# Kernel tuning notes

Hardware: AMD Instinct MI355X
Metric: run time of the kernel (lower is better)

The kernel has to match this reference:

```python
import jax, jax.numpy as jnp
import numpy as np

# Production dims: NTU-RGB+D skeletons, mid-network AGCN block
N, C, T, V = 64, 64, 300, 25   # batch, channels, frames, joints
S = 3                          # num_subset (spatial partitions of adjacency)
IC = 64 // 4                   # inter_channels = out_channels // coff_embedding
OC = 64                        # out_channels (== in_channels -> down is Identity)
BN_EPS = 1e-5


def setup_inputs() -> dict:
    key = jax.random.key(0)
    ks = jax.random.split(key, 13)
    x = jax.random.normal(ks[0], (N, C, T, V), jnp.float32)
    A = jax.random.uniform(ks[1], (S, V, V), jnp.float32)          # fixed graph buffer
    PA = jax.random.normal(ks[2], (S, V, V), jnp.float32) * 1e-3   # learned adjacency (init ~1e-6)
    wa = jax.random.normal(ks[3], (S, IC, C), jnp.float32) * 0.05  # conv_a 1x1 weights
    ba = jax.random.normal(ks[4], (S, IC), jnp.float32) * 0.01
    wb = jax.random.normal(ks[5], (S, IC, C), jnp.float32) * 0.05  # conv_b 1x1 weights
    bb = jax.random.normal(ks[6], (S, IC), jnp.float32) * 0.01
    wd = jax.random.normal(ks[7], (S, OC, C), jnp.float32) * 0.05  # conv_d 1x1 weights
    bd = jax.random.normal(ks[8], (S, OC), jnp.float32) * 0.01
    bn_gamma = jax.random.uniform(ks[9], (OC,), jnp.float32) + 0.5
    bn_beta = jax.random.normal(ks[10], (OC,), jnp.float32) * 0.1
    bn_mean = jax.random.normal(ks[11], (OC,), jnp.float32) * 0.1
    bn_var = jax.random.uniform(ks[12], (OC,), jnp.float32) + 0.5
    return {"x": x, "A": A, "PA": PA, "wa": wa, "ba": ba, "wb": wb, "bb": bb,
            "wd": wd, "bd": bd, "bn_gamma": bn_gamma, "bn_beta": bn_beta,
            "bn_mean": bn_mean, "bn_var": bn_var}


def reference(x, A, PA, wa, ba, wb, bb, wd, bd, bn_gamma, bn_beta, bn_mean, bn_var):
    n, c, t, v = x.shape
    s, ic, _ = wa.shape
    A_total = A + PA                                                # (S,V,V)

    # conv_a / conv_b are 1x1 convs over channels, vectorized over subsets
    a = jnp.einsum('nctv,skc->nsktv', x, wa) + ba[None, :, :, None, None]  # (N,S,IC,T,V)
    b = jnp.einsum('nctv,skc->nsktv', x, wb) + bb[None, :, :, None, None]

    # attention_a: permute(0,3,1,2).view(N, V, IC*T); attention_b: view(N, IC*T, V)
    a_flat = a.transpose(0, 1, 4, 2, 3).reshape(n, s, v, ic * t)   # (N,S,V,IC*T)
    b_flat = b.reshape(n, s, ic * t, v)                            # (N,S,IC*T,V)

    scores = jnp.einsum('nsvm,nsmu->nsvu', a_flat, b_flat) / (ic * t)
    att = jax.nn.softmax(scores, axis=-2) + A_total[None]          # softmax over dim -2, then + adjacency

    # feature matmul: x.view(N, C*T, V) @ att  ==  contract over node axis v
    y = jnp.einsum('nctv,nsvu->nsctu', x, att)                     # (N,S,C,T,V)
    # conv_d (1x1) per subset, summed over subsets
    z = jnp.einsum('nsctv,soc->notv', y, wd) + jnp.sum(bd, axis=0)[None, :, None, None]

    # BatchNorm2d (inference form with running stats)
    scale = (bn_gamma / jnp.sqrt(bn_var + BN_EPS))[None, :, None, None]
    zn = (z - bn_mean[None, :, None, None]) * scale + bn_beta[None, :, None, None]

    # down is Identity since in_channels == out_channels
    return jax.nn.relu(zn + x)
```

## Files before the change

### kernel.cpp

```cpp
#include <hip/hip_runtime.h>
#include <math.h>


typedef short  short4v  __attribute__((ext_vector_type(4)));
typedef short  short8v  __attribute__((ext_vector_type(8)));
typedef float  float4v  __attribute__((ext_vector_type(4)));

#define MFMA_BF16(a,b,c) __builtin_amdgcn_mfma_f32_16x16x32_bf16((a),(b),(c),0,0,0)

__device__ __forceinline__ unsigned short f2bf(float f) {
  union { float f; unsigned int u; } v; v.f = f;
  unsigned int r = v.u + 0x7FFFu + ((v.u >> 16) & 1u);
  return (unsigned short)(r >> 16);
}
__device__ __forceinline__ unsigned pack2bf(float a, float b) {
#if __has_builtin(__builtin_amdgcn_cvt_pk_bf16_f32)
  typedef __bf16 bf2_t __attribute__((ext_vector_type(2)));
  bf2_t p = __builtin_amdgcn_cvt_pk_bf16_f32(a, b);
  union { bf2_t v; unsigned u; } c; c.v = p; return c.u;
#else
  return (unsigned)f2bf(a) | ((unsigned)f2bf(b) << 16);
#endif
}
__device__ __forceinline__ short8v pk8(const float* f) {
  union { unsigned u[4]; short8v s; } c;
  c.u[0] = pack2bf(f[0], f[1]); c.u[1] = pack2bf(f[2], f[3]);
  c.u[2] = pack2bf(f[4], f[5]); c.u[3] = pack2bf(f[6], f[7]);
  return c.s;
}
__device__ __forceinline__ short8v ld8_b64(const unsigned short* p) {
  short4v a = *(const short4v*)p;
  short4v b = *(const short4v*)(p + 4);
  short8v r;
  r[0]=a[0]; r[1]=a[1]; r[2]=a[2]; r[3]=a[3];
  r[4]=b[0]; r[5]=b[1]; r[6]=b[2]; r[7]=b[3];
  return r;
}

__global__ __launch_bounds__(256) void k0_zero(float* __restrict__ p, int nelem) {
  int i = blockIdx.x * 256 + threadIdx.x;
  if (i < nelem) p[i] = 0.f;
}

__global__ __launch_bounds__(256) void k1_scores(
    const float* __restrict__ x,  const float* __restrict__ wa,
    const float* __restrict__ ba, const float* __restrict__ wb,
    const float* __restrict__ bb, float* __restrict__ scores)
{
  __shared__ __align__(16) unsigned short ET[3][160*40];
  const unsigned tid  = threadIdx.x;
  const unsigned lane = tid & 63u, w = tid >> 6;
  const unsigned l15  = lane & 15u, q = lane >> 4;
  const unsigned n = blockIdx.y, ts = blockIdx.x;
  const unsigned t0 = ts * 12u;
  const float* xn = x + (size_t)n * 480000;

  short8v Wf[3][2][2];
  #pragma unroll
  for (int s = 0; s < 3; ++s)
    #pragma unroll
    for (int mt = 0; mt < 2; ++mt)
      #pragma unroll
      for (int ks = 0; ks < 2; ++ks) {
        const float* src = (mt ? wb : wa) + ((size_t)s*16 + l15)*64
                         + (unsigned)ks*32 + q*8;
        float tf[8];
        #pragma unroll
        for (int j = 0; j < 8; ++j) tf[j] = src[j];
        Wf[s][mt][ks] = pk8(tf);
      }
  float bias[3][2][4];
  #pragma unroll
  for (int s = 0; s < 3; ++s)
    #pragma unroll
    for (int mt = 0; mt < 2; ++mt)
      #pragma unroll
      for (int r = 0; r < 4; ++r)
        bias[s][mt][r] = (mt ? bb : ba)[s*16 + q*4 + (unsigned)r];

  float4v acc[3];
  #pragma unroll
  for (int j = 0; j < 3; ++j) acc[j] = (float4v){0.f,0.f,0.f,0.f};

  for (unsigned ch = 0; ch < 2; ++ch) {
    const unsigned tvbase = (t0 + ch*6u) * 25u;
    if (ch) __syncthreads();
    for (unsigned nn = 0; nn < 3; ++nn) {
      unsigned nt = w + 4*nn;
      if (nt < 10) {
        unsigned tvb = nt*16 + l15;
        unsigned tvg = tvbase + tvb;
        if (tvg > 7499u) tvg = 7499u;
        const float* p = xn + (size_t)q*60000 + tvg;
        float xa[8], xb[8];
        #pragma unroll
        for (int j = 0; j < 8; ++j) {
          xa[j] = p[(size_t)j*7500];
          xb[j] = p[240000 + (size_t)j*7500];
        }
        short8v B0 = pk8(xa), B1 = pk8(xb);
        #pragma unroll
        for (int s = 0; s < 3; ++s)
          #pragma unroll
          for (int mt = 0; mt < 2; ++mt) {
            float4v d = (float4v){0.f,0.f,0.f,0.f};
            d = MFMA_BF16(Wf[s][mt][0], B0, d);
            d = MFMA_BF16(Wf[s][mt][1], B1, d);
            unsigned krb = (unsigned)mt*16 + q*4;
            uint2 pk2;
            pk2.x = pack2bf(d[0] + bias[s][mt][0], d[1] + bias[s][mt][1]);
            pk2.y = pack2bf(d[2] + bias[s][mt][2], d[3] + bias[s][mt][3]);
            *(uint2*)(&ET[s][tvb*40 + krb]) = pk2;
          }
      }
    }
    __syncthreads();
    #pragma unroll
    for (int j = 0; j < 3; ++j) {
      unsigned g = (unsigned)j*4 + w;
      unsigned s = g >> 2, mt = (g >> 1) & 1u, nt2 = g & 1u;
      #pragma unroll
      for (int ks = 0; ks < 3; ++ks) {
        unsigned t    = 2*ks + (q >> 1);
        unsigned kofs = 8*(q & 1u);
        short8v Af = *(const short8v*)(&ET[s][(t*25 + mt*16  + l15)*40 + kofs]);
        short8v Bf = *(const short8v*)(&ET[s][(t*25 + nt2*16 + l15)*40 + 16 + kofs]);
        acc[j] = MFMA_BF16(Af, Bf, acc[j]);
      }
    }
  }
  #pragma unroll
  for (int j = 0; j < 3; ++j) {
    unsigned g = (unsigned)j*4 + w;
    unsigned s = g >> 2, mt = (g >> 1) & 1u, nt2 = g & 1u;
    unsigned u = nt2*16 + l15;
    if (u < 25) {
      #pragma unroll
      for (int r = 0; r < 4; ++r) {
        unsigned v = mt*16 + q*4 + (unsigned)r;
        if (v < 25)
          atomicAdd(&scores[(size_t)n*1875 + s*625 + v*25 + u], acc[j][r]);
      }
    }
  }
}

__global__ __launch_bounds__(64) void k2_softmax(
    const float* __restrict__ scores, const float* __restrict__ A,
    const float* __restrict__ PA, float* __restrict__ att)
{
  const unsigned tid = threadIdx.x, s = blockIdx.x, n = blockIdx.y;
  if (tid >= 25) return;
  const unsigned u = tid;
  float col[25];
  float m = -1e30f;
  #pragma unroll
  for (int v = 0; v < 25; ++v) {
    col[v] = scores[(size_t)n*1875 + s*625 + (unsigned)v*25 + u] * (1.f/4800.f);
    m = fmaxf(m, col[v]);
  }
  float S = 0.f;
  #pragma unroll
  for (int v = 0; v < 25; ++v) { col[v] = expf(col[v] - m); S += col[v]; }
  float inv = 1.f / S;
  #pragma unroll
  for (int v = 0; v < 25; ++v)
    att[(((size_t)n*3 + s)*25 + (unsigned)v)*25 + u] =
        col[v]*inv + A[s*625 + (unsigned)v*25 + u] + PA[s*625 + (unsigned)v*25 + u];
}

__global__ __launch_bounds__(256) void k3_main(
    const float* __restrict__ x,   const float* __restrict__ wd,
    const float* __restrict__ bd,  const float* __restrict__ gam,
    const float* __restrict__ bet, const float* __restrict__ mu,
    const float* __restrict__ var, const float* __restrict__ att,
    float* __restrict__ out)
{
  __shared__ __align__(16) unsigned short Pt[2][32*196];
  const unsigned tid  = threadIdx.x;
  const unsigned lane = tid & 63u, mt = tid >> 6;
  const unsigned l15  = lane & 15u, q = lane >> 4;
  const unsigned n = blockIdx.y, t0 = blockIdx.x * 10u;

  float ksr[4], kbr[4];
  #pragma unroll
  for (int r = 0; r < 4; ++r) {
    unsigned o = mt*16 + q*4 + (unsigned)r;
    float sc = gam[o] * rsqrtf(var[o] + 1e-5f);
    ksr[r] = sc;
    kbr[r] = (bd[o] + bd[64+o] + bd[128+o] - mu[o]) * sc + bet[o];
  }
  short8v ATf[3][2];
  #pragma unroll
  for (int s = 0; s < 3; ++s)
    #pragma unroll
    for (int nt2 = 0; nt2 < 2; ++nt2) {
      unsigned u = (unsigned)nt2*16 + l15;
      float tf[8];
      #pragma unroll
      for (int j = 0; j < 8; ++j) {
        unsigned v = q*8 + (unsigned)j;
        tf[j] = (v < 25 && u < 25) ? att[(((size_t)n*3 + s)*25 + v)*25 + u] : 0.f;
      }
      ATf[s][nt2] = pk8(tf);
    }
  short8v Awf[6];
  #pragma unroll
  for (int ks = 0; ks < 6; ++ks) {
    const float* src = wd + ((size_t)((unsigned)ks>>1)*64 + mt*16 + l15)*64
                     + ((unsigned)ks & 1u)*32 + q*8;
    float tf[8];
    #pragma unroll
    for (int j = 0; j < 8; ++j) tf[j] = src[j];
    Awf[ks] = pk8(tf);
  }
  unsigned offs[2][4];
  const bool valid1 = (l15 < 9);
  #pragma unroll
  for (int nt2 = 0; nt2 < 2; ++nt2)
    #pragma unroll
    for (int r = 0; r < 4; ++r)
      offs[nt2][r] = (mt*16 + q*4 + (unsigned)r)*7500u + (unsigned)nt2*16 + l15;

  const float* xn = x + (size_t)n * 480000;
  float*       on = (float*)out + (size_t)n * 480000;
  const float* xr = xn + (size_t)(mt*16 + l15)*7500;

  {
    const float* pa = xr + t0*25 + q*8;
    float fa[8];
    #pragma unroll
    for (int j = 0; j < 8; ++j) fa[j] = pa[j];
    short8v Ax = pk8(fa);
    #pragma unroll
    for (int s = 0; s < 3; ++s)
      #pragma unroll
      for (int nt2 = 0; nt2 < 2; ++nt2) {
        float4v d = (float4v){0.f,0.f,0.f,0.f};
        d = MFMA_BF16(Ax, ATf[s][nt2], d);
        unsigned u  = (unsigned)nt2*16 + l15;
        unsigned kb = (unsigned)s*64 + mt*16 + q*4;
        uint2 pk2; pk2.x = pack2bf(d[0], d[1]); pk2.y = pack2bf(d[2], d[3]);
        *(uint2*)(&Pt[0][u*196 + kb]) = pk2;
      }
  }

  for (unsigned t = 0; t < 10; ++t) {
    const unsigned cur = t & 1u, nxt = cur ^ 1u;
    const unsigned tg = t0 + t, t25 = tg*25;
    __syncthreads();

    const bool hasnext = (t + 1u < 10u);
    short8v Axn;
    if (hasnext) {
      const float* pa = xr + t25 + 25 + q*8;
      float fa[8];
      #pragma unroll
      for (int j = 0; j < 8; ++j) fa[j] = pa[j];
      Axn = pk8(fa);
    }
    float xv[2][4];
    #pragma unroll
    for (int nt2 = 0; nt2 < 2; ++nt2)
      if (nt2 == 0 || valid1) {
        #pragma unroll
        for (int r = 0; r < 4; ++r) xv[nt2][r] = xn[offs[nt2][r] + t25];
      }
    float4v za = (float4v){0.f,0.f,0.f,0.f}, zb = (float4v){0.f,0.f,0.f,0.f};
    #pragma unroll
    for (int ks = 0; ks < 6; ++ks) {
      short8v B0 = ld8_b64(&Pt[cur][l15*196      + (unsigned)ks*32 + q*8]);
      short8v B1 = ld8_b64(&Pt[cur][(16+l15)*196 + (unsigned)ks*32 + q*8]);
      za = MFMA_BF16(Awf[ks], B0, za);
      zb = MFMA_BF16(Awf[ks], B1, zb);
    }
    if (hasnext) {
      #pragma unroll
      for (int s = 0; s < 3; ++s)
        #pragma unroll
        for (int nt2 = 0; nt2 < 2; ++nt2) {
          float4v d = (float4v){0.f,0.f,0.f,0.f};
          d = MFMA_BF16(Axn, ATf[s][nt2], d);
          unsigned u  = (unsigned)nt2*16 + l15;
          unsigned kb = (unsigned)s*64 + mt*16 + q*4;
          uint2 pk2; pk2.x = pack2bf(d[0], d[1]); pk2.y = pack2bf(d[2], d[3]);
          *(uint2*)(&Pt[nxt][u*196 + kb]) = pk2;
        }
    }
    #pragma unroll
    for (int nt2 = 0; nt2 < 2; ++nt2) {
      float4v zz = nt2 ? zb : za;
      if (nt2 == 0 || valid1) {
        #pragma unroll
        for (int r = 0; r < 4; ++r) {
          float val = zz[r]*ksr[r] + kbr[r] + xv[nt2][r];
          on[offs[nt2][r] + t25] = fmaxf(val, 0.f);
        }
      }
    }
  }
}

extern "C" void kernel_launch(void* const* d_in, const int* in_sizes, int n_in,
                              void* d_out, int out_size, void* d_ws, size_t ws_size,
                              hipStream_t stream)
{
  (void)in_sizes; (void)n_in; (void)out_size; (void)ws_size;
  const float* x   = (const float*)d_in[0];
  const float* A   = (const float*)d_in[1];
  const float* PA  = (const float*)d_in[2];
  const float* wa  = (const float*)d_in[3];
  const float* ba  = (const float*)d_in[4];
  const float* wb  = (const float*)d_in[5];
  const float* bb  = (const float*)d_in[6];
  const float* wd  = (const float*)d_in[7];
  const float* bd  = (const float*)d_in[8];
  const float* gam = (const float*)d_in[9];
  const float* bet = (const float*)d_in[10];
  const float* mu  = (const float*)d_in[11];
  const float* var = (const float*)d_in[12];
  float* out    = (float*)d_out;
  float* scores = (float*)d_ws;
  float* att    = scores + 120000;

  hipLaunchKernelGGL(k0_zero, dim3((120000 + 255)/256), dim3(256), 0, stream,
                     scores, 120000);
  hipLaunchKernelGGL(k1_scores, dim3(25, 64), dim3(256), 0, stream,
                     x, wa, ba, wb, bb, scores);
  hipLaunchKernelGGL(k2_softmax, dim3(3, 64), dim3(64), 0, stream,
                     scores, A, PA, att);
  hipLaunchKernelGGL(k3_main, dim3(30, 64), dim3(256), 0, stream,
                     x, wd, bd, gam, bet, mu, var, att, out);
}
```

Measured before the change: 323.4 us.

## Replace score atomics with partial slabs, remap k3 grid for XCDs, prefetch loads

```diff
diff --git a/kernel.cpp b/kernel.cpp
--- a/kernel.cpp
+++ b/kernel.cpp
@@ -45,7 +45,8 @@
 __global__ __launch_bounds__(256) void k1_scores(
     const float* __restrict__ x,  const float* __restrict__ wa,
     const float* __restrict__ ba, const float* __restrict__ wb,
-    const float* __restrict__ bb, float* __restrict__ scores)
+    const float* __restrict__ bb, float* __restrict__ scores,
+    float* __restrict__ part,     int use_atomic)
 {
   __shared__ __align__(16) unsigned short ET[3][160*40];
   const unsigned tid  = threadIdx.x;
@@ -129,17 +130,35 @@
       }
     }
   }
-  #pragma unroll
-  for (int j = 0; j < 3; ++j) {
-    unsigned g = (unsigned)j*4 + w;
-    unsigned s = g >> 2, mt = (g >> 1) & 1u, nt2 = g & 1u;
-    unsigned u = nt2*16 + l15;
-    if (u < 25) {
-      #pragma unroll
-      for (int r = 0; r < 4; ++r) {
-        unsigned v = mt*16 + q*4 + (unsigned)r;
-        if (v < 25)
-          atomicAdd(&scores[(size_t)n*1875 + s*625 + v*25 + u], acc[j][r]);
+  if (use_atomic) {
+    #pragma unroll
+    for (int j = 0; j < 3; ++j) {
+      unsigned g = (unsigned)j*4 + w;
+      unsigned s = g >> 2, mt = (g >> 1) & 1u, nt2 = g & 1u;
+      unsigned u = nt2*16 + l15;
+      if (u < 25) {
+        #pragma unroll
+        for (int r = 0; r < 4; ++r) {
+          unsigned v = mt*16 + q*4 + (unsigned)r;
+          if (v < 25)
+            atomicAdd(&scores[(size_t)n*1875 + s*625 + v*25 + u], acc[j][r]);
+        }
+      }
+    }
+  } else {
+    float* slab = part + ((size_t)ts*64u + n)*1875u;
+    #pragma unroll
+    for (int j = 0; j < 3; ++j) {
+      unsigned g = (unsigned)j*4 + w;
+      unsigned s = g >> 2, mt = (g >> 1) & 1u, nt2 = g & 1u;
+      unsigned u = nt2*16 + l15;
+      if (u < 25) {
+        #pragma unroll
+        for (int r = 0; r < 4; ++r) {
+          unsigned v = mt*16 + q*4 + (unsigned)r;
+          if (v < 25)
+            slab[s*625u + v*25u + u] = acc[j][r];
+        }
       }
     }
   }
@@ -169,7 +188,41 @@
         col[v]*inv + A[s*625 + (unsigned)v*25 + u] + PA[s*625 + (unsigned)v*25 + u];
 }
 
-__global__ __launch_bounds__(256) void k3_main(
+__global__ __launch_bounds__(256) void k2_softmax_r(
+    const float* __restrict__ part, const float* __restrict__ A,
+    const float* __restrict__ PA, float* __restrict__ att)
+{
+  __shared__ float sm[625];
+  const unsigned tid = threadIdx.x, s = blockIdx.x, n = blockIdx.y;
+  for (unsigned cell = tid; cell < 625u; cell += 256u) {
+    float acc = 0.f;
+    #pragma unroll
+    for (int ts = 0; ts < 25; ++ts)
+      acc += part[((size_t)ts*64u + n)*1875u + s*625u + cell];
+    sm[cell] = acc;
+  }
+  __syncthreads();
+  if (tid < 25) {
+    const unsigned u = tid;
+    float col[25];
+    float m = -1e30f;
+    #pragma unroll
+    for (int v = 0; v < 25; ++v) {
+      col[v] = sm[(unsigned)v*25 + u] * (1.f/4800.f);
+      m = fmaxf(m, col[v]);
+    }
+    float S = 0.f;
+    #pragma unroll
+    for (int v = 0; v < 25; ++v) { col[v] = expf(col[v] - m); S += col[v]; }
+    float inv = 1.f / S;
+    #pragma unroll
+    for (int v = 0; v < 25; ++v)
+      att[(((size_t)n*3 + s)*25 + (unsigned)v)*25 + u] =
+          col[v]*inv + A[s*625 + (unsigned)v*25 + u] + PA[s*625 + (unsigned)v*25 + u];
+  }
+}
+
+__global__ __launch_bounds__(256, 4) void k3_main(
     const float* __restrict__ x,   const float* __restrict__ wd,
     const float* __restrict__ bd,  const float* __restrict__ gam,
     const float* __restrict__ bet, const float* __restrict__ mu,
@@ -180,7 +233,10 @@
   const unsigned tid  = threadIdx.x;
   const unsigned lane = tid & 63u, mt = tid >> 6;
   const unsigned l15  = lane & 15u, q = lane >> 4;
-  const unsigned n = blockIdx.y, t0 = blockIdx.x * 10u;
+  const unsigned wid = blockIdx.x;
+  const unsigned xcd = wid & 7u, li = wid >> 3;
+  const unsigned n   = xcd + 8u*(li/20u);
+  const unsigned t0  = (li % 20u) * 15u;
 
   float ksr[4], kbr[4];
   #pragma unroll
@@ -244,28 +300,43 @@
         *(uint2*)(&Pt[0][u*196 + kb]) = pk2;
       }
   }
-
-  for (unsigned t = 0; t < 10; ++t) {
-    const unsigned cur = t & 1u, nxt = cur ^ 1u;
-    const unsigned tg = t0 + t, t25 = tg*25;
+  float aN[8];
+  {
+    const float* pa = xr + t0*25 + 25 + q*8;
+    #pragma unroll
+    for (int j = 0; j < 8; ++j) aN[j] = pa[j];
+  }
+  float xvC[2][4];
+  #pragma unroll
+  for (int nt2 = 0; nt2 < 2; ++nt2)
+    if (nt2 == 0 || valid1) {
+      #pragma unroll
+      for (int r = 0; r < 4; ++r) xvC[nt2][r] = xn[offs[nt2][r] + t0*25];
+    }
+
+  #pragma unroll
+  for (int t = 0; t < 15; ++t) {
+    const unsigned cur = (unsigned)t & 1u, nxt = cur ^ 1u;
+    const unsigned t25 = (t0 + (unsigned)t)*25u;
     __syncthreads();
 
-    const bool hasnext = (t + 1u < 10u);
-    short8v Axn;
-    if (hasnext) {
-      const float* pa = xr + t25 + 25 + q*8;
-      float fa[8];
-      #pragma unroll
-      for (int j = 0; j < 8; ++j) fa[j] = pa[j];
-      Axn = pk8(fa);
-    }
-    float xv[2][4];
-    #pragma unroll
-    for (int nt2 = 0; nt2 < 2; ++nt2)
-      if (nt2 == 0 || valid1) {
-        #pragma unroll
-        for (int r = 0; r < 4; ++r) xv[nt2][r] = xn[offs[nt2][r] + t25];
-      }
+    const bool pfA = (t < 13);
+    const bool pfR = (t < 14);
+    float aP[8];
+    float xvN[2][4];
+    if (pfA) {
+      const float* pa = xr + t25 + 50 + q*8;
+      #pragma unroll
+      for (int j = 0; j < 8; ++j) aP[j] = pa[j];
+    }
+    if (pfR) {
+      #pragma unroll
+      for (int nt2 = 0; nt2 < 2; ++nt2)
+        if (nt2 == 0 || valid1) {
+          #pragma unroll
+          for (int r = 0; r < 4; ++r) xvN[nt2][r] = xn[offs[nt2][r] + t25 + 25u];
+        }
+    }
     float4v za = (float4v){0.f,0.f,0.f,0.f}, zb = (float4v){0.f,0.f,0.f,0.f};
     #pragma unroll
     for (int ks = 0; ks < 6; ++ks) {
@@ -274,13 +345,14 @@
       za = MFMA_BF16(Awf[ks], B0, za);
       zb = MFMA_BF16(Awf[ks], B1, zb);
     }
-    if (hasnext) {
+    if (t < 14) {
+      short8v Ax = pk8(aN);
       #pragma unroll
       for (int s = 0; s < 3; ++s)
         #pragma unroll
         for (int nt2 = 0; nt2 < 2; ++nt2) {
           float4v d = (float4v){0.f,0.f,0.f,0.f};
-          d = MFMA_BF16(Axn, ATf[s][nt2], d);
+          d = MFMA_BF16(Ax, ATf[s][nt2], d);
           unsigned u  = (unsigned)nt2*16 + l15;
           unsigned kb = (unsigned)s*64 + mt*16 + q*4;
           uint2 pk2; pk2.x = pack2bf(d[0], d[1]); pk2.y = pack2bf(d[2], d[3]);
@@ -293,10 +365,20 @@
       if (nt2 == 0 || valid1) {
         #pragma unroll
         for (int r = 0; r < 4; ++r) {
-          float val = zz[r]*ksr[r] + kbr[r] + xv[nt2][r];
-          on[offs[nt2][r] + t25] = fmaxf(val, 0.f);
-        }
-      }
+          float val = zz[r]*ksr[r] + kbr[r] + xvC[nt2][r];
+          __builtin_nontemporal_store(fmaxf(val, 0.f), &on[offs[nt2][r] + t25]);
+        }
+      }
+    }
+    if (pfA) {
+      #pragma unroll
+      for (int j = 0; j < 8; ++j) aN[j] = aP[j];
+    }
+    if (pfR) {
+      #pragma unroll
+      for (int nt2 = 0; nt2 < 2; ++nt2)
+        #pragma unroll
+        for (int r = 0; r < 4; ++r) xvC[nt2][r] = xvN[nt2][r];
     }
   }
 }
@@ -305,7 +387,7 @@
                               void* d_out, int out_size, void* d_ws, size_t ws_size,
                               hipStream_t stream)
 {
-  (void)in_sizes; (void)n_in; (void)out_size; (void)ws_size;
+  (void)in_sizes; (void)n_in; (void)out_size;
   const float* x   = (const float*)d_in[0];
   const float* A   = (const float*)d_in[1];
   const float* PA  = (const float*)d_in[2];
@@ -319,16 +401,28 @@
   const float* bet = (const float*)d_in[10];
   const float* mu  = (const float*)d_in[11];
   const float* var = (const float*)d_in[12];
-  float* out    = (float*)d_out;
-  float* scores = (float*)d_ws;
-  float* att    = scores + 120000;
-
-  hipLaunchKernelGGL(k0_zero, dim3((120000 + 255)/256), dim3(256), 0, stream,
-                     scores, 120000);
-  hipLaunchKernelGGL(k1_scores, dim3(25, 64), dim3(256), 0, stream,
-                     x, wa, ba, wb, bb, scores);
-  hipLaunchKernelGGL(k2_softmax, dim3(3, 64), dim3(64), 0, stream,
-                     scores, A, PA, att);
-  hipLaunchKernelGGL(k3_main, dim3(30, 64), dim3(256), 0, stream,
-                     x, wd, bd, gam, bet, mu, var, att, out);
-}
+  float* out = (float*)d_out;
+
+  const size_t NEED = (size_t)(25*120000 + 120000) * sizeof(float);
+  if (ws_size >= NEED) {
+    float* part = (float*)d_ws;
+    float* att  = part + 3000000;
+    hipLaunchKernelGGL(k1_scores, dim3(25, 64), dim3(256), 0, stream,
+                       x, wa, ba, wb, bb, part, part, 0);
+    hipLaunchKernelGGL(k2_softmax_r, dim3(3, 64), dim3(256), 0, stream,
+                       part, A, PA, att);
+    hipLaunchKernelGGL(k3_main, dim3(1280), dim3(256), 0, stream,
+                       x, wd, bd, gam, bet, mu, var, att, out);
+  } else {
+    float* scores = (float*)d_ws;
+    float* att    = scores + 120000;
+    hipLaunchKernelGGL(k0_zero, dim3((120000 + 255)/256), dim3(256), 0, stream,
+                       scores, 120000);
+    hipLaunchKernelGGL(k1_scores, dim3(25, 64), dim3(256), 0, stream,
+                       x, wa, ba, wb, bb, scores, scores, 1);
+    hipLaunchKernelGGL(k2_softmax, dim3(3, 64), dim3(64), 0, stream,
+                       scores, A, PA, att);
+    hipLaunchKernelGGL(k3_main, dim3(1280), dim3(256), 0, stream,
+                       x, wd, bd, gam, bet, mu, var, att, out);
+  }
+}
```

After: 470.5 us. 45.5% more time.
